# Kernel tuning notes

Measured on AMD Instinct MI355X. Metric: run time of the kernel, lower is better.

Reference implementation:

```python
import jax, jax.numpy as jnp
import numpy as np
from itertools import combinations

NDIM = 256
BATCH = 65536


def setup_inputs() -> dict:
    key = jax.random.key(0)
    k1, k2 = jax.random.split(key)
    pairs = np.array(list(combinations(range(NDIM), 2)), dtype=np.int32)  # [comb(ndim,2), 2]
    return {
        "x": jax.random.normal(k1, (BATCH, NDIM), dtype=jnp.float32),
        "rots": jax.random.normal(k2, (pairs.shape[0],), dtype=jnp.float32),
        "idx_i": jnp.asarray(pairs[:, 0]),
        "idx_j": jnp.asarray(pairs[:, 1]),
    }


def _build_mat(rots, idx_i, idx_j, ndim):
    # Equivalent to mat = R_last @ ... @ R_first @ I, then return mat.T.
    # Each Givens rotation R_(i,j,theta) only mixes rows i and j, so we update
    # two rows per step (O(ndim) work) instead of a dense ndim x ndim matmul.
    # Torch uses cfloat, but all imaginary parts are identically zero, so
    # float32 computes the same math.
    def step(mat, t):
        i, j, theta = t
        c = jnp.cos(theta)
        s = jnp.sin(theta)
        ri = mat[i]
        rj = mat[j]
        mat = mat.at[i].set(c * ri - s * rj)
        mat = mat.at[j].set(s * ri + c * rj)
        return mat, None

    mat0 = jnp.eye(ndim, dtype=rots.dtype)
    mat, _ = jax.lax.scan(step, mat0, (idx_i, idx_j, rots))
    return mat.T  # forward does x @ mat.T


def reference(x, rots, idx_i, idx_j):
    m = _build_mat(rots, idx_i, idx_j, x.shape[-1])  # [ndim, ndim]
    return x @ m
```

## Files before the change

### kernel.cpp

```cpp
#include <hip/hip_runtime.h>
#include <hip/hip_bf16.h>

#define NDIM 256
#define NROT 32640
#define NSEG 64
#define SEGLEN 510
#define MATE (NDIM * NDIM)

typedef __bf16 bf16x4_t __attribute__((ext_vector_type(4)));
typedef __bf16 bf16x8_t __attribute__((ext_vector_type(8)));
typedef float f32x4_t __attribute__((ext_vector_type(4)));

__global__ void k_sincos(const float* __restrict__ rots, float2* __restrict__ cs) {
    int k = blockIdx.x * 256 + threadIdx.x;
    if (k < NROT) {
        float th = rots[k];
        float s, c;
        sincosf(th, &s, &c);
        cs[k] = make_float2(c, s);
    }
}

__global__ __launch_bounds__(64, 1) void k_build(const float2* __restrict__ cs,
                                                 float* __restrict__ leaves) {
    __shared__ float tile[NDIM * 64];
    __shared__ float2 csl[SEGLEN + 8];
    const int t = threadIdx.x;
    const int seg = blockIdx.x >> 2;
    const int cg = blockIdx.x & 3;
    const int col = cg * 64 + t;

    const float2* csg = cs + (size_t)seg * SEGLEN;
    for (int u = t; u < SEGLEN + 8; u += 64) csl[u] = csg[u];

    for (int r = 0; r < NDIM; r++) tile[r * 64 + t] = (r == col) ? 1.0f : 0.0f;

    int k = 0;
    const int kg0 = seg * SEGLEN;
    int i = 0, cum = 0;
    while (cum + (NDIM - 1 - i) <= kg0) { cum += NDIM - 1 - i; i++; }
    int j = i + 1 + (kg0 - cum);

    while (k < SEGLEN) {
        float ri = tile[i * 64 + t];
        const int len = min(NDIM - j, SEGLEN - k);
        const int jend = j + len;
        const int nb = len >> 3;

        if (nb > 0) {
            float2 cv[8]; float rj[8];
            #pragma unroll
            for (int u = 0; u < 8; u++) cv[u] = csl[k + u];
            #pragma unroll
            for (int u = 0; u < 8; u++) rj[u] = tile[(j + u) * 64 + t];
            for (int b = 0; b < nb - 1; b++) {
                float2 cvn[8]; float rjn[8];
                #pragma unroll
                for (int u = 0; u < 8; u++) cvn[u] = csl[k + 8 + u];
                #pragma unroll
                for (int u = 0; u < 8; u++) rjn[u] = tile[(j + 8 + u) * 64 + t];
                #pragma unroll
                for (int u = 0; u < 8; u++) {
                    float nri = fmaf(cv[u].x, ri, -(cv[u].y * rj[u]));
                    rj[u]     = fmaf(cv[u].y, ri,  cv[u].x * rj[u]);
                    ri = nri;
                }
                #pragma unroll
                for (int u = 0; u < 8; u++) tile[(j + u) * 64 + t] = rj[u];
                #pragma unroll
                for (int u = 0; u < 8; u++) { cv[u] = cvn[u]; rj[u] = rjn[u]; }
                j += 8; k += 8;
            }
            #pragma unroll
            for (int u = 0; u < 8; u++) {
                float nri = fmaf(cv[u].x, ri, -(cv[u].y * rj[u]));
                rj[u]     = fmaf(cv[u].y, ri,  cv[u].x * rj[u]);
                ri = nri;
            }
            #pragma unroll
            for (int u = 0; u < 8; u++) tile[(j + u) * 64 + t] = rj[u];
            j += 8; k += 8;
        }
        for (; j < jend; j++, k++) {
            float2 cv = csl[k];
            float rj = tile[j * 64 + t];
            float nri = fmaf(cv.x, ri, -(cv.y * rj));
            tile[j * 64 + t] = fmaf(cv.y, ri, cv.x * rj);
            ri = nri;
        }
        tile[i * 64 + t] = ri;
        if (j == NDIM) { i++; j = i + 1; }
    }

    float* dst = leaves + (size_t)seg * MATE;
    if (seg & 1) {
        for (int r = 0; r < NDIM; r++)
            dst[r * NDIM + col] = tile[r * 64 + t];
    } else {
        for (int r0 = 0; r0 < NDIM; r0 += 4) {
            f32x4_t v = {tile[(r0 + 0) * 64 + t], tile[(r0 + 1) * 64 + t],
                         tile[(r0 + 2) * 64 + t], tile[(r0 + 3) * 64 + t]};
            *(f32x4_t*)&dst[(size_t)col * NDIM + r0] = v;
        }
    }
}

#define LDB 40
__global__ __launch_bounds__(256) void k_combine(const float* __restrict__ src,
                                                 float* __restrict__ dst,
                                                 int finalLevel) {
    const int p = blockIdx.x >> 2;
    const int quad = blockIdx.x & 3;
    const int rb = (quad >> 1) * 128;
    const int cb = (quad & 1) * 128;
    const float* A = src + (size_t)(2 * p) * MATE;
    const float* B = src + (size_t)(2 * p + 1) * MATE;
    float* C = dst + (size_t)p * MATE;
    const bool storeT = (!finalLevel) && ((p & 1) == 0);
    const int t = threadIdx.x;
    const int wid = t >> 6, lane = t & 63;
    const int wro = (wid >> 1) * 64, wco = (wid & 1) * 64;
    const int lrow = lane & 15, kg = lane >> 4;

    __shared__ __bf16 Bhi[128 * LDB];
    __shared__ __bf16 Blo[128 * LDB];
    __shared__ __bf16 Ahi[128 * LDB];
    __shared__ __bf16 Alo[128 * LDB];

    f32x4_t acc[4][4] = {};

    for (int kc = 0; kc < NDIM; kc += 32) {
        __syncthreads();
        #pragma unroll
        for (int qq = 0; qq < 4; qq++) {
            int fi = t + qq * 256;
            int row = fi >> 3, sg = fi & 7;
            f32x4_t vb = *(const f32x4_t*)&B[(size_t)(rb + row) * NDIM + kc + sg * 4];
            f32x4_t va = *(const f32x4_t*)&A[(size_t)(cb + row) * NDIM + kc + sg * 4];
            bf16x4_t bh = {(__bf16)vb.x, (__bf16)vb.y, (__bf16)vb.z, (__bf16)vb.w};
            bf16x4_t ah = {(__bf16)va.x, (__bf16)va.y, (__bf16)va.z, (__bf16)va.w};
            bf16x4_t bl = {(__bf16)(vb.x - (float)bh[0]), (__bf16)(vb.y - (float)bh[1]),
                           (__bf16)(vb.z - (float)bh[2]), (__bf16)(vb.w - (float)bh[3])};
            bf16x4_t al = {(__bf16)(va.x - (float)ah[0]), (__bf16)(va.y - (float)ah[1]),
                           (__bf16)(va.z - (float)ah[2]), (__bf16)(va.w - (float)ah[3])};
            *(bf16x4_t*)&Bhi[row * LDB + sg * 4] = bh;
            *(bf16x4_t*)&Blo[row * LDB + sg * 4] = bl;
            *(bf16x4_t*)&Ahi[row * LDB + sg * 4] = ah;
            *(bf16x4_t*)&Alo[row * LDB + sg * 4] = al;
        }
        __syncthreads();

        bf16x8_t afh[4], afl[4], bfh[4], bfl[4];
        #pragma unroll
        for (int mt = 0; mt < 4; mt++) {
            afh[mt] = *(const bf16x8_t*)&Bhi[(wro + mt * 16 + lrow) * LDB + kg * 8];
            afl[mt] = *(const bf16x8_t*)&Blo[(wro + mt * 16 + lrow) * LDB + kg * 8];
        }
        #pragma unroll
        for (int nt = 0; nt < 4; nt++) {
            bfh[nt] = *(const bf16x8_t*)&Ahi[(wco + nt * 16 + lrow) * LDB + kg * 8];
            bfl[nt] = *(const bf16x8_t*)&Alo[(wco + nt * 16 + lrow) * LDB + kg * 8];
        }
        #pragma unroll
        for (int mt = 0; mt < 4; mt++)
            #pragma unroll
            for (int nt = 0; nt < 4; nt++) {
                acc[mt][nt] = __builtin_amdgcn_mfma_f32_16x16x32_bf16(afh[mt], bfh[nt], acc[mt][nt], 0, 0, 0);
                acc[mt][nt] = __builtin_amdgcn_mfma_f32_16x16x32_bf16(afh[mt], bfl[nt], acc[mt][nt], 0, 0, 0);
                acc[mt][nt] = __builtin_amdgcn_mfma_f32_16x16x32_bf16(afl[mt], bfh[nt], acc[mt][nt], 0, 0, 0);
            }
    }

    if (storeT) {
        #pragma unroll
        for (int mt = 0; mt < 4; mt++)
            #pragma unroll
            for (int nt = 0; nt < 4; nt++) {
                int gr = rb + wro + mt * 16 + kg * 4;
                int gc = cb + wco + nt * 16 + lrow;
                *(f32x4_t*)&C[(size_t)gc * NDIM + gr] = acc[mt][nt];
            }
    } else {
        #pragma unroll
        for (int mt = 0; mt < 4; mt++)
            #pragma unroll
            for (int nt = 0; nt < 4; nt++)
                #pragma unroll
                for (int r = 0; r < 4; r++)
                    C[(size_t)(rb + wro + mt * 16 + kg * 4 + r) * NDIM
                      + cb + wco + nt * 16 + lrow] = acc[mt][nt][r];
    }
}

#define LD 40
__global__ __launch_bounds__(256, 3) void k_gemm(const float* __restrict__ X,
                                                 const float* __restrict__ Mmat,
                                                 float* __restrict__ Y) {
    __shared__ __bf16 As[128 * LD];
    __shared__ __bf16 Bs[128 * LD];
    const int bx = blockIdx.x;
    const int xcd = bx & 7;
    const int q = bx >> 3;
    const int bn = (q & 1) * 128;
    const int bm = (xcd + (q >> 1) * 8) * 128;
    const int t = threadIdx.x;
    const int wid = t >> 6;
    const int lane = t & 63;
    const int wr = (wid >> 1) * 64;
    const int wc = (wid & 1) * 64;
    const int lrow = lane & 15;
    const int kg = lane >> 4;

    f32x4_t acc[4][4] = {};

    for (int kc = 0; kc < 256; kc += 32) {
        __syncthreads();
        #pragma unroll
        for (int qq = 0; qq < 4; qq++) {
            int fi = t + qq * 256;
            int row = fi >> 3, sg = fi & 7;
            f32x4_t v = *(const f32x4_t*)&X[(size_t)(bm + row) * 256 + kc + sg * 4];
            bf16x4_t h = {(__bf16)v.x, (__bf16)v.y, (__bf16)v.z, (__bf16)v.w};
            *(bf16x4_t*)&As[row * LD + sg * 4] = h;
        }
        #pragma unroll
        for (int qq = 0; qq < 4; qq++) {
            int fi = t + qq * 256;
            int row = fi >> 3, sg = fi & 7;
            f32x4_t v = *(const f32x4_t*)&Mmat[(size_t)(bn + row) * 256 + kc + sg * 4];
            bf16x4_t h = {(__bf16)v.x, (__bf16)v.y, (__bf16)v.z, (__bf16)v.w};
            *(bf16x4_t*)&Bs[row * LD + sg * 4] = h;
        }
        __syncthreads();

        bf16x8_t af[4], bfr[4];
        #pragma unroll
        for (int mt = 0; mt < 4; mt++)
            af[mt] = *(const bf16x8_t*)&As[(wr + mt * 16 + lrow) * LD + kg * 8];
        #pragma unroll
        for (int nt = 0; nt < 4; nt++)
            bfr[nt] = *(const bf16x8_t*)&Bs[(wc + nt * 16 + lrow) * LD + kg * 8];
        #pragma unroll
        for (int mt = 0; mt < 4; mt++)
            #pragma unroll
            for (int nt = 0; nt < 4; nt++)
                acc[mt][nt] = __builtin_amdgcn_mfma_f32_16x16x32_bf16(af[mt], bfr[nt], acc[mt][nt], 0, 0, 0);
    }

    const int ocol = bn + wc + lrow;
    const int orow = bm + wr + kg * 4;
    #pragma unroll
    for (int mt = 0; mt < 4; mt++)
        #pragma unroll
        for (int nt = 0; nt < 4; nt++)
            #pragma unroll
            for (int r = 0; r < 4; r++)
                Y[(size_t)(orow + mt * 16 + r) * 256 + ocol + nt * 16] = acc[mt][nt][r];
}

extern "C" void kernel_launch(void* const* d_in, const int* in_sizes, int n_in,
                              void* d_out, int out_size, void* d_ws, size_t ws_size,
                              hipStream_t stream) {
    const float* x = (const float*)d_in[0];
    const float* rots = (const float*)d_in[1];
    float* out = (float*)d_out;

    char* wsb = (char*)d_ws;
    float2* cs = (float2*)wsb;
    float* B0 = (float*)(wsb + 262144);
    float* B1 = B0 + (size_t)NSEG * MATE;

    k_sincos<<<128, 256, 0, stream>>>(rots, cs);
    k_build<<<NSEG * 4, 64, 0, stream>>>(cs, B0);
    k_combine<<<32 * 4, 256, 0, stream>>>(B0, B1, 0);
    k_combine<<<16 * 4, 256, 0, stream>>>(B1, B0, 0);
    k_combine<<<8 * 4, 256, 0, stream>>>(B0, B1, 0);
    k_combine<<<4 * 4, 256, 0, stream>>>(B1, B0, 0);
    k_combine<<<2 * 4, 256, 0, stream>>>(B0, B1, 0);
    k_combine<<<1 * 4, 256, 0, stream>>>(B1, B0, 1);
    k_gemm<<<1024, 256, 0, stream>>>(x, B0, out);
}
```

Before: 264.9 us.

## Fuse sincos into build, store bf16 hi/lo splits, retile combine and pipeline gemm

Moves sincos into the build kernel, so one launch and the cos/sin round-trip through global memory go away. Leaves and intermediate products are now stored as pre-split bf16 hi/lo planes instead of fp32, which halves bytes moved and drops the per-tile splitting work in combine. Combine now uses 64x64 output tiles with the full K dimension staged once in LDS, giving 16 blocks per pair for more parallelism at the small tree levels. The final GEMM uses a 64-wide K step with register prefetch of the next chunk during MFMA, and the final matrix is read directly as bf16. Occupancy drops to 2 blocks per CU because of the larger LDS tiles.

```diff
diff --git a/kernel.cpp b/kernel.cpp
--- a/kernel.cpp
+++ b/kernel.cpp
@@ -1,28 +1,20 @@
 #include <hip/hip_runtime.h>
 #include <hip/hip_bf16.h>
+#include <math.h>
 
 #define NDIM 256
 #define NROT 32640
 #define NSEG 64
 #define SEGLEN 510
 #define MATE (NDIM * NDIM)
+#define NODEE (2 * MATE)
 
 typedef __bf16 bf16x4_t __attribute__((ext_vector_type(4)));
 typedef __bf16 bf16x8_t __attribute__((ext_vector_type(8)));
 typedef float f32x4_t __attribute__((ext_vector_type(4)));
 
-__global__ void k_sincos(const float* __restrict__ rots, float2* __restrict__ cs) {
-    int k = blockIdx.x * 256 + threadIdx.x;
-    if (k < NROT) {
-        float th = rots[k];
-        float s, c;
-        sincosf(th, &s, &c);
-        cs[k] = make_float2(c, s);
-    }
-}
-
-__global__ __launch_bounds__(64, 1) void k_build(const float2* __restrict__ cs,
-                                                 float* __restrict__ leaves) {
+__global__ __launch_bounds__(64, 1) void k_build(const float* __restrict__ rots,
+                                                 __bf16* __restrict__ leaves) {
     __shared__ float tile[NDIM * 64];
     __shared__ float2 csl[SEGLEN + 8];
     const int t = threadIdx.x;
@@ -30,13 +22,18 @@
     const int cg = blockIdx.x & 3;
     const int col = cg * 64 + t;
 
-    const float2* csg = cs + (size_t)seg * SEGLEN;
-    for (int u = t; u < SEGLEN + 8; u += 64) csl[u] = csg[u];
+    const int kg0 = seg * SEGLEN;
+    for (int u = t; u < SEGLEN; u += 64) {
+        float th = rots[kg0 + u];
+        float s, c;
+        sincosf(th, &s, &c);
+        csl[u] = make_float2(c, s);
+    }
+    for (int u = SEGLEN + t; u < SEGLEN + 8; u += 64) csl[u] = make_float2(1.f, 0.f);
 
     for (int r = 0; r < NDIM; r++) tile[r * 64 + t] = (r == col) ? 1.0f : 0.0f;
 
     int k = 0;
-    const int kg0 = seg * SEGLEN;
     int i = 0, cum = 0;
     while (cum + (NDIM - 1 - i) <= kg0) { cum += NDIM - 1 - i; i++; }
     int j = i + 1 + (kg0 - cum);
@@ -92,112 +89,130 @@
         if (j == NDIM) { i++; j = i + 1; }
     }
 
-    float* dst = leaves + (size_t)seg * MATE;
+    __bf16* hi = leaves + (size_t)seg * NODEE;
+    __bf16* lo = hi + MATE;
     if (seg & 1) {
-        for (int r = 0; r < NDIM; r++)
-            dst[r * NDIM + col] = tile[r * 64 + t];
+        for (int r = 0; r < NDIM; r++) {
+            float v = tile[r * 64 + t];
+            __bf16 h = (__bf16)v;
+            hi[r * NDIM + col] = h;
+            lo[r * NDIM + col] = (__bf16)(v - (float)h);
+        }
     } else {
-        for (int r0 = 0; r0 < NDIM; r0 += 4) {
-            f32x4_t v = {tile[(r0 + 0) * 64 + t], tile[(r0 + 1) * 64 + t],
-                         tile[(r0 + 2) * 64 + t], tile[(r0 + 3) * 64 + t]};
-            *(f32x4_t*)&dst[(size_t)col * NDIM + r0] = v;
+        for (int r0 = 0; r0 < NDIM; r0 += 8) {
+            bf16x8_t vh, vl;
+            #pragma unroll
+            for (int u = 0; u < 8; u++) {
+                float v = tile[(r0 + u) * 64 + t];
+                __bf16 h = (__bf16)v;
+                vh[u] = h;
+                vl[u] = (__bf16)(v - (float)h);
+            }
+            *(bf16x8_t*)&hi[(size_t)col * NDIM + r0] = vh;
+            *(bf16x8_t*)&lo[(size_t)col * NDIM + r0] = vl;
         }
     }
 }
 
-#define LDB 40
-__global__ __launch_bounds__(256) void k_combine(const float* __restrict__ src,
-                                                 float* __restrict__ dst,
+#define LDK 264
+__global__ __launch_bounds__(256) void k_combine(const __bf16* __restrict__ src,
+                                                 __bf16* __restrict__ dst,
                                                  int finalLevel) {
-    const int p = blockIdx.x >> 2;
-    const int quad = blockIdx.x & 3;
-    const int rb = (quad >> 1) * 128;
-    const int cb = (quad & 1) * 128;
-    const float* A = src + (size_t)(2 * p) * MATE;
-    const float* B = src + (size_t)(2 * p + 1) * MATE;
-    float* C = dst + (size_t)p * MATE;
+    __shared__ __bf16 planes[4][64 * LDK];
+
+    const int p = blockIdx.x >> 4;
+    const int qd = blockIdx.x & 15;
+    const int rbq = (qd >> 2) * 64;
+    const int cbq = (qd & 3) * 64;
+    const __bf16* A = src + (size_t)(2 * p) * NODEE;
+    const __bf16* B = src + (size_t)(2 * p + 1) * NODEE;
+    __bf16* Chi = dst + (size_t)p * NODEE;
+    __bf16* Clo = Chi + MATE;
     const bool storeT = (!finalLevel) && ((p & 1) == 0);
+
     const int t = threadIdx.x;
     const int wid = t >> 6, lane = t & 63;
-    const int wro = (wid >> 1) * 64, wco = (wid & 1) * 64;
+    const int wr2 = (wid >> 1) * 32, wc2 = (wid & 1) * 32;
     const int lrow = lane & 15, kg = lane >> 4;
 
-    __shared__ __bf16 Bhi[128 * LDB];
-    __shared__ __bf16 Blo[128 * LDB];
-    __shared__ __bf16 Ahi[128 * LDB];
-    __shared__ __bf16 Alo[128 * LDB];
-
-    f32x4_t acc[4][4] = {};
-
-    for (int kc = 0; kc < NDIM; kc += 32) {
-        __syncthreads();
-        #pragma unroll
-        for (int qq = 0; qq < 4; qq++) {
-            int fi = t + qq * 256;
-            int row = fi >> 3, sg = fi & 7;
-            f32x4_t vb = *(const f32x4_t*)&B[(size_t)(rb + row) * NDIM + kc + sg * 4];
-            f32x4_t va = *(const f32x4_t*)&A[(size_t)(cb + row) * NDIM + kc + sg * 4];
-            bf16x4_t bh = {(__bf16)vb.x, (__bf16)vb.y, (__bf16)vb.z, (__bf16)vb.w};
-            bf16x4_t ah = {(__bf16)va.x, (__bf16)va.y, (__bf16)va.z, (__bf16)va.w};
-            bf16x4_t bl = {(__bf16)(vb.x - (float)bh[0]), (__bf16)(vb.y - (float)bh[1]),
-                           (__bf16)(vb.z - (float)bh[2]), (__bf16)(vb.w - (float)bh[3])};
-            bf16x4_t al = {(__bf16)(va.x - (float)ah[0]), (__bf16)(va.y - (float)ah[1]),
-                           (__bf16)(va.z - (float)ah[2]), (__bf16)(va.w - (float)ah[3])};
-            *(bf16x4_t*)&Bhi[row * LDB + sg * 4] = bh;
-            *(bf16x4_t*)&Blo[row * LDB + sg * 4] = bl;
-            *(bf16x4_t*)&Ahi[row * LDB + sg * 4] = ah;
-            *(bf16x4_t*)&Alo[row * LDB + sg * 4] = al;
-        }
-        __syncthreads();
-
-        bf16x8_t afh[4], afl[4], bfh[4], bfl[4];
-        #pragma unroll
-        for (int mt = 0; mt < 4; mt++) {
-            afh[mt] = *(const bf16x8_t*)&Bhi[(wro + mt * 16 + lrow) * LDB + kg * 8];
-            afl[mt] = *(const bf16x8_t*)&Blo[(wro + mt * 16 + lrow) * LDB + kg * 8];
-        }
-        #pragma unroll
-        for (int nt = 0; nt < 4; nt++) {
-            bfh[nt] = *(const bf16x8_t*)&Ahi[(wco + nt * 16 + lrow) * LDB + kg * 8];
-            bfl[nt] = *(const bf16x8_t*)&Alo[(wco + nt * 16 + lrow) * LDB + kg * 8];
-        }
-        #pragma unroll
-        for (int mt = 0; mt < 4; mt++)
-            #pragma unroll
-            for (int nt = 0; nt < 4; nt++) {
+    const __bf16* plane_src[4] = {B, B + MATE, A, A + MATE};
+    const int plane_row0[4] = {rbq, rbq, cbq, cbq};
+    #pragma unroll
+    for (int q = 0; q < 32; q++) {
+        int g = q * 256 + t;
+        int pl = g >> 11;
+        int c = g & 2047;
+        int row = c >> 5, sg = c & 31;
+        bf16x8_t v = *(const bf16x8_t*)&plane_src[pl][(size_t)(plane_row0[pl] + row) * NDIM + sg * 8];
+        *(bf16x8_t*)&planes[pl][row * LDK + sg * 8] = v;
+    }
+    __syncthreads();
+
+    f32x4_t acc[2][2] = {};
+    #pragma unroll
+    for (int kc = 0; kc < 8; kc++) {
+        bf16x8_t afh[2], afl[2], bfh[2], bfl[2];
+        #pragma unroll
+        for (int mt = 0; mt < 2; mt++) {
+            int r = (wr2 + mt * 16 + lrow) * LDK + kc * 32 + kg * 8;
+            afh[mt] = *(const bf16x8_t*)&planes[0][r];
+            afl[mt] = *(const bf16x8_t*)&planes[1][r];
+        }
+        #pragma unroll
+        for (int nt = 0; nt < 2; nt++) {
+            int r = (wc2 + nt * 16 + lrow) * LDK + kc * 32 + kg * 8;
+            bfh[nt] = *(const bf16x8_t*)&planes[2][r];
+            bfl[nt] = *(const bf16x8_t*)&planes[3][r];
+        }
+        #pragma unroll
+        for (int mt = 0; mt < 2; mt++)
+            #pragma unroll
+            for (int nt = 0; nt < 2; nt++) {
                 acc[mt][nt] = __builtin_amdgcn_mfma_f32_16x16x32_bf16(afh[mt], bfh[nt], acc[mt][nt], 0, 0, 0);
                 acc[mt][nt] = __builtin_amdgcn_mfma_f32_16x16x32_bf16(afh[mt], bfl[nt], acc[mt][nt], 0, 0, 0);
                 acc[mt][nt] = __builtin_amdgcn_mfma_f32_16x16x32_bf16(afl[mt], bfh[nt], acc[mt][nt], 0, 0, 0);
             }
     }
 
-    if (storeT) {
-        #pragma unroll
-        for (int mt = 0; mt < 4; mt++)
-            #pragma unroll
-            for (int nt = 0; nt < 4; nt++) {
-                int gr = rb + wro + mt * 16 + kg * 4;
-                int gc = cb + wco + nt * 16 + lrow;
-                *(f32x4_t*)&C[(size_t)gc * NDIM + gr] = acc[mt][nt];
-            }
-    } else {
-        #pragma unroll
-        for (int mt = 0; mt < 4; mt++)
-            #pragma unroll
-            for (int nt = 0; nt < 4; nt++)
+    #pragma unroll
+    for (int mt = 0; mt < 2; mt++)
+        #pragma unroll
+        for (int nt = 0; nt < 2; nt++) {
+            int grow = rbq + wr2 + mt * 16 + kg * 4;
+            int gcol = cbq + wc2 + nt * 16 + lrow;
+            if (storeT) {
+                bf16x4_t vh, vl;
+                #pragma unroll
+                for (int r = 0; r < 4; r++) {
+                    float v = acc[mt][nt][r];
+                    __bf16 h = (__bf16)v;
+                    vh[r] = h;
+                    vl[r] = (__bf16)(v - (float)h);
+                }
+                *(bf16x4_t*)&Chi[(size_t)gcol * NDIM + grow] = vh;
+                *(bf16x4_t*)&Clo[(size_t)gcol * NDIM + grow] = vl;
+            } else if (finalLevel) {
                 #pragma unroll
                 for (int r = 0; r < 4; r++)
-                    C[(size_t)(rb + wro + mt * 16 + kg * 4 + r) * NDIM
-                      + cb + wco + nt * 16 + lrow] = acc[mt][nt][r];
-    }
+                    Chi[(size_t)(grow + r) * NDIM + gcol] = (__bf16)acc[mt][nt][r];
+            } else {
+                #pragma unroll
+                for (int r = 0; r < 4; r++) {
+                    float v = acc[mt][nt][r];
+                    __bf16 h = (__bf16)v;
+                    Chi[(size_t)(grow + r) * NDIM + gcol] = h;
+                    Clo[(size_t)(grow + r) * NDIM + gcol] = (__bf16)(v - (float)h);
+                }
+            }
+        }
 }
 
-#define LD 40
-__global__ __launch_bounds__(256, 3) void k_gemm(const float* __restrict__ X,
-                                                 const float* __restrict__ Mmat,
+#define LDA 72
+__global__ __launch_bounds__(256, 2) void k_gemm(const float* __restrict__ X,
+                                                 const __bf16* __restrict__ Mhi,
                                                  float* __restrict__ Y) {
-    __shared__ __bf16 As[128 * LD];
-    __shared__ __bf16 Bs[128 * LD];
+    __shared__ __bf16 As[128 * LDA];
+    __shared__ __bf16 Bs[128 * LDA];
     const int bx = blockIdx.x;
     const int xcd = bx & 7;
     const int q = bx >> 3;
@@ -213,38 +228,66 @@
 
     f32x4_t acc[4][4] = {};
 
-    for (int kc = 0; kc < 256; kc += 32) {
+    f32x4_t ra[8];
+    bf16x8_t rb[4];
+
+    #pragma unroll
+    for (int qq = 0; qq < 8; qq++) {
+        int g = qq * 256 + t;
+        ra[qq] = *(const f32x4_t*)&X[(size_t)(bm + (g >> 4)) * 256 + (g & 15) * 4];
+    }
+    #pragma unroll
+    for (int qq = 0; qq < 4; qq++) {
+        int g = qq * 256 + t;
+        rb[qq] = *(const bf16x8_t*)&Mhi[(size_t)(bn + (g >> 3)) * 256 + (g & 7) * 8];
+    }
+
+    #pragma unroll
+    for (int it = 0; it < 4; it++) {
+        #pragma unroll
+        for (int qq = 0; qq < 8; qq++) {
+            int g = qq * 256 + t;
+            f32x4_t v = ra[qq];
+            bf16x4_t h = {(__bf16)v.x, (__bf16)v.y, (__bf16)v.z, (__bf16)v.w};
+            *(bf16x4_t*)&As[(g >> 4) * LDA + (g & 15) * 4] = h;
+        }
+        #pragma unroll
+        for (int qq = 0; qq < 4; qq++) {
+            int g = qq * 256 + t;
+            *(bf16x8_t*)&Bs[(g >> 3) * LDA + (g & 7) * 8] = rb[qq];
+        }
         __syncthreads();
-        #pragma unroll
-        for (int qq = 0; qq < 4; qq++) {
-            int fi = t + qq * 256;
-            int row = fi >> 3, sg = fi & 7;
-            f32x4_t v = *(const f32x4_t*)&X[(size_t)(bm + row) * 256 + kc + sg * 4];
-            bf16x4_t h = {(__bf16)v.x, (__bf16)v.y, (__bf16)v.z, (__bf16)v.w};
-            *(bf16x4_t*)&As[row * LD + sg * 4] = h;
-        }
-        #pragma unroll
-        for (int qq = 0; qq < 4; qq++) {
-            int fi = t + qq * 256;
-            int row = fi >> 3, sg = fi & 7;
-            f32x4_t v = *(const f32x4_t*)&Mmat[(size_t)(bn + row) * 256 + kc + sg * 4];
-            bf16x4_t h = {(__bf16)v.x, (__bf16)v.y, (__bf16)v.z, (__bf16)v.w};
-            *(bf16x4_t*)&Bs[row * LD + sg * 4] = h;
+
+        if (it < 3) {
+            int kc = (it + 1) * 64;
+            #pragma unroll
+            for (int qq = 0; qq < 8; qq++) {
+                int g = qq * 256 + t;
+                ra[qq] = *(const f32x4_t*)&X[(size_t)(bm + (g >> 4)) * 256 + kc + (g & 15) * 4];
+            }
+            #pragma unroll
+            for (int qq = 0; qq < 4; qq++) {
+                int g = qq * 256 + t;
+                rb[qq] = *(const bf16x8_t*)&Mhi[(size_t)(bn + (g >> 3)) * 256 + kc + (g & 7) * 8];
+            }
+        }
+
+        #pragma unroll
+        for (int k2 = 0; k2 < 2; k2++) {
+            bf16x8_t af[4], bfr[4];
+            #pragma unroll
+            for (int mt = 0; mt < 4; mt++)
+                af[mt] = *(const bf16x8_t*)&As[(wr + mt * 16 + lrow) * LDA + k2 * 32 + kg * 8];
+            #pragma unroll
+            for (int nt = 0; nt < 4; nt++)
+                bfr[nt] = *(const bf16x8_t*)&Bs[(wc + nt * 16 + lrow) * LDA + k2 * 32 + kg * 8];
+            #pragma unroll
+            for (int mt = 0; mt < 4; mt++)
+                #pragma unroll
+                for (int nt = 0; nt < 4; nt++)
+                    acc[mt][nt] = __builtin_amdgcn_mfma_f32_16x16x32_bf16(af[mt], bfr[nt], acc[mt][nt], 0, 0, 0);
         }
         __syncthreads();
-
-        bf16x8_t af[4], bfr[4];
-        #pragma unroll
-        for (int mt = 0; mt < 4; mt++)
-            af[mt] = *(const bf16x8_t*)&As[(wr + mt * 16 + lrow) * LD + kg * 8];
-        #pragma unroll
-        for (int nt = 0; nt < 4; nt++)
-            bfr[nt] = *(const bf16x8_t*)&Bs[(wc + nt * 16 + lrow) * LD + kg * 8];
-        #pragma unroll
-        for (int mt = 0; mt < 4; mt++)
-            #pragma unroll
-            for (int nt = 0; nt < 4; nt++)
-                acc[mt][nt] = __builtin_amdgcn_mfma_f32_16x16x32_bf16(af[mt], bfr[nt], acc[mt][nt], 0, 0, 0);
     }
 
     const int ocol = bn + wc + lrow;
@@ -265,18 +308,15 @@
     const float* rots = (const float*)d_in[1];
     float* out = (float*)d_out;
 
-    char* wsb = (char*)d_ws;
-    float2* cs = (float2*)wsb;
-    float* B0 = (float*)(wsb + 262144);
-    float* B1 = B0 + (size_t)NSEG * MATE;
-
-    k_sincos<<<128, 256, 0, stream>>>(rots, cs);
-    k_build<<<NSEG * 4, 64, 0, stream>>>(cs, B0);
-    k_combine<<<32 * 4, 256, 0, stream>>>(B0, B1, 0);
-    k_combine<<<16 * 4, 256, 0, stream>>>(B1, B0, 0);
-    k_combine<<<8 * 4, 256, 0, stream>>>(B0, B1, 0);
-    k_combine<<<4 * 4, 256, 0, stream>>>(B1, B0, 0);
-    k_combine<<<2 * 4, 256, 0, stream>>>(B0, B1, 0);
-    k_combine<<<1 * 4, 256, 0, stream>>>(B1, B0, 1);
+    __bf16* B0 = (__bf16*)d_ws;
+    __bf16* B1 = B0 + (size_t)NSEG * NODEE;
+
+    k_build<<<NSEG * 4, 64, 0, stream>>>(rots, B0);
+    k_combine<<<32 * 16, 256, 0, stream>>>(B0, B1, 0);
+    k_combine<<<16 * 16, 256, 0, stream>>>(B1, B0, 0);
+    k_combine<<<8 * 16, 256, 0, stream>>>(B0, B1, 0);
+    k_combine<<<4 * 16, 256, 0, stream>>>(B1, B0, 0);
+    k_combine<<<2 * 16, 256, 0, stream>>>(B0, B1, 0);
+    k_combine<<<1 * 16, 256, 0, stream>>>(B1, B0, 1);
     k_gemm<<<1024, 256, 0, stream>>>(x, B0, out);
 }
```

Measured after the change: 228.5 us. 1.16x faster.
